# Kernel optimization log

Measured on AMD Instinct MI355X. Metric: run time of the kernel, lower is better.

The kernel has to match this reference:

```python
import jax, jax.numpy as jnp
import numpy as np
from jax.scipy.special import erfc

CUTOFF = 10.0   # real-space cutoff (Angstrom)
ALPHA = 0.3     # Ewald splitting parameter (1/Angstrom)
KMAX = 8        # max integer k-index per dimension
N_ATOMS = 4096
BOX = 40.0      # cubic box edge (Angstrom)


def setup_inputs() -> dict:
    key = jax.random.key(0)
    kp, kq = jax.random.split(key)
    positions = jax.random.uniform(kp, (N_ATOMS, 3), dtype=jnp.float32) * BOX
    charges = jax.random.normal(kq, (N_ATOMS,), dtype=jnp.float32)
    charges = charges - charges.mean()  # enforce charge neutrality
    cell = jnp.eye(3, dtype=jnp.float32) * BOX  # row-vector lattice
    return {"positions": positions, "charges": charges, "cell": cell}


def _kvectors(kmax):
    # static integer grid (-kmax..kmax)^3 \\ {0}, built with numpy at trace time
    n = np.arange(-kmax, kmax + 1)
    grid = np.stack(np.meshgrid(n, n, n, indexing="ij"), axis=-1).reshape(-1, 3)
    grid = grid[np.any(grid != 0, axis=-1)]
    return jnp.asarray(grid, dtype=jnp.float32)  # [Nk, 3]


def _ewald(positions, charges, cell, cutoff, alpha, kmax):
    N = positions.shape[0]
    inv_cell = jnp.linalg.inv(cell)

    # ---- real-space sum: 0.5 * sum_{i!=j, r<rc} q_i q_j erfc(a r)/r (min image)
    rij = positions[:, None, :] - positions[None, :, :]          # [N,N,3]
    frac = rij @ inv_cell
    rij = (frac - jnp.round(frac)) @ cell                        # minimum image
    r2 = jnp.sum(rij * rij, axis=-1)                             # [N,N]
    eye = jnp.eye(N, dtype=bool)
    r = jnp.sqrt(jnp.where(eye, 1.0, r2))                        # safe sqrt on diag
    pair_mask = (~eye) & (r2 < cutoff * cutoff)
    qq = charges[:, None] * charges[None, :]
    e_real = 0.5 * jnp.sum(jnp.where(pair_mask, qq * erfc(alpha * r) / r, 0.0))

    # ---- reciprocal-space sum: (2pi/V) sum_k exp(-k^2/4a^2)/k^2 |S(k)|^2
    recip = 2.0 * jnp.pi * inv_cell.T                            # reciprocal lattice rows
    kvecs = _kvectors(kmax) @ recip                              # [Nk,3]
    k2 = jnp.sum(kvecs * kvecs, axis=-1)                         # [Nk]
    phase = positions @ kvecs.T                                  # [N,Nk]
    s_re = charges @ jnp.cos(phase)                              # [Nk]
    s_im = charges @ jnp.sin(phase)                              # [Nk]
    vol = jnp.abs(jnp.linalg.det(cell))
    coeff = jnp.exp(-k2 / (4.0 * alpha * alpha)) / k2
    e_recip = (2.0 * jnp.pi / vol) * jnp.sum(coeff * (s_re * s_re + s_im * s_im))

    # ---- self-energy correction
    e_self = -(alpha / jnp.sqrt(jnp.pi)) * jnp.sum(charges * charges)

    return e_real + e_recip + e_self


def reference(positions, charges, cell):
    return _ewald(positions, charges, cell, CUTOFF, ALPHA, KMAX)
```

## Files before the change

kernel.cpp:

```cpp
#include <hip/hip_runtime.h>
#include <math.h>

#define ALPHA 0.3f
#define KMAX 8
#define KDIM 17
#define KD2 (KDIM*KDIM)
#define NK_FULL (KDIM*KDIM*KDIM - 1)
#define NK_HALF (NK_FULL/2)
#define RECIP_KB ((NK_HALF + 255)/256)
#define KPAD (RECIP_KB*256)
#define RECIP_CHUNKS 16
#define TWO_PI 6.28318530717958647692f

#define SELF_COEF (-0.16925687506432687f)
#define INV_4A2 (1.0f/(4.0f*ALPHA*ALPHA))
#define C1A (0.3275911f*ALPHA)
#define NA2 (-(ALPHA*ALPHA))

#define ITILE 512
#define JTILE 32

__device__ __forceinline__ void invert3x3(const float* __restrict__ c, float inv[9], float* det_out) {
    float a00=c[0],a01=c[1],a02=c[2];
    float a10=c[3],a11=c[4],a12=c[5];
    float a20=c[6],a21=c[7],a22=c[8];
    float c00 =  a11*a22 - a12*a21;
    float c01 = -(a10*a22 - a12*a20);
    float c02 =  a10*a21 - a11*a20;
    float det = a00*c00 + a01*c01 + a02*c02;
    float id = 1.0f/det;
    inv[0] =  c00*id;
    inv[1] = -(a01*a22 - a02*a21)*id;
    inv[2] =  (a01*a12 - a02*a11)*id;
    inv[3] =  c01*id;
    inv[4] =  (a00*a22 - a02*a20)*id;
    inv[5] = -(a00*a12 - a02*a10)*id;
    inv[6] =  c02*id;
    inv[7] = -(a00*a21 - a01*a20)*id;
    inv[8] =  (a00*a11 - a01*a10)*id;
    *det_out = det;
}

__device__ __forceinline__ float erfc_a(float r, float r2) {
    float t = __builtin_amdgcn_rcpf(fmaf(C1A, r, 1.0f));
    float p = t * fmaf(t, fmaf(t, fmaf(t, fmaf(t, 1.061405429f, -1.453152027f),
                       1.421413741f), -0.284496736f), 0.254829592f);
    return p * __expf(NA2 * r2);
}

__device__ __forceinline__ float block_reduce(float v) {
    for (int o = 32; o > 0; o >>= 1) v += __shfl_down(v, o, 64);
    __shared__ float smem[4];
    int lane = threadIdx.x & 63, wid = threadIdx.x >> 6;
    if (lane == 0) smem[wid] = v;
    __syncthreads();
    int nw = (blockDim.x + 63) >> 6;
    v = ((int)threadIdx.x < nw) ? smem[threadIdx.x] : 0.0f;
    if (wid == 0) {
        for (int o = 4; o > 0; o >>= 1) v += __shfl_down(v, o, 64);
    }
    return v;
}

__global__ __launch_bounds__(256) void fused_kernel(const float* __restrict__ pos,
                                                    const float* __restrict__ q,
                                                    const float* __restrict__ cell,
                                                    float* __restrict__ spart,
                                                    float* __restrict__ rpart,
                                                    int N, int nb_recip) {
    float inv[9]; float det;
    invert3x3(cell, inv, &det);
    bool ortho = (cell[1]==0.f) & (cell[2]==0.f) & (cell[3]==0.f) &
                 (cell[5]==0.f) & (cell[6]==0.f) & (cell[7]==0.f);
    bool cubic = ortho & (cell[0]==cell[4]) & (cell[0]==cell[8]);

    int bid = blockIdx.x;
    int tid = threadIdx.x;

    if (bid < nb_recip) {
        __shared__ float4 atile[256];
        int kb    = bid % RECIP_KB;
        int chunk = bid / RECIP_KB;
        int k = kb * 256 + tid;
        bool kvalid = (k < NK_HALF);
        int kk = kvalid ? k : 0;
        float kx = (float)(kk / KD2 - KMAX);
        float ky = (float)((kk / KDIM) % KDIM - KMAX);
        float kz = (float)(kk % KDIM - KMAX);

        int per = (N + RECIP_CHUNKS - 1) / RECIP_CHUNKS;
        int a0 = chunk * per;
        int a1 = min(N, a0 + per);

        float sre = 0.0f, sim = 0.0f;
        for (int base = a0; base < a1; base += 256) {
            int cnt = min(256, a1 - base);
            __syncthreads();
            if (tid < cnt) {
                int a = base + tid;
                float x = pos[3*a], y = pos[3*a+1], z = pos[3*a+2];
                float wx, wy, wz;
                if (ortho) { wx = x*inv[0]; wy = y*inv[4]; wz = z*inv[8]; }
                else {
                    wx = inv[0]*x + inv[3]*y + inv[6]*z;
                    wy = inv[1]*x + inv[4]*y + inv[7]*z;
                    wz = inv[2]*x + inv[5]*y + inv[8]*z;
                }
                atile[tid] = make_float4(wx, wy, wz, q[a]);
            }
            __syncthreads();
            #pragma unroll 4
            for (int t = 0; t < cnt; ++t) {
                float4 w = atile[t];
                float ph = fmaf(kx, w.x, fmaf(ky, w.y, kz * w.z));
                ph -= rintf(ph);
                sre = fmaf(w.w, __builtin_amdgcn_cosf(ph), sre);
                sim = fmaf(w.w, __builtin_amdgcn_sinf(ph), sim);
            }
        }
        spart[(size_t)(chunk*2    ) * KPAD + k] = kvalid ? sre : 0.0f;
        spart[(size_t)(chunk*2 + 1) * KPAD + k] = kvalid ? sim : 0.0f;
    } else {
        __shared__ float4 tile[JTILE];
        int rbid = bid - nb_recip;
        int bi = 0, acc = 0;
        for (;;) {
            int up = min(N, (bi + 1) * ITILE);
            int nc = (up + JTILE - 1) / JTILE;
            if (rbid < acc + nc) break;
            acc += nc; ++bi;
        }
        int bj = rbid - acc;

        int ibase = bi * ITILE;
        int jbase = bj * JTILE;
        int jcount = min(JTILE, N - jbase);

        int i1 = ibase + tid;
        int i2 = i1 + 256;
        bool v1 = (i1 < N), v2 = (i2 < N);

        float L = cell[0], invL = inv[0];
        float C1AL = C1A * L;
        float NBL  = NA2 * L * L;

        float x1=0.f,y1=0.f,z1=0.f,q1=0.f, x2=0.f,y2=0.f,z2=0.f,q2=0.f;

        if (cubic) {
            if (v1) { x1 = pos[3*i1]*invL; y1 = pos[3*i1+1]*invL; z1 = pos[3*i1+2]*invL; q1 = q[i1]; }
            if (v2) { x2 = pos[3*i2]*invL; y2 = pos[3*i2+1]*invL; z2 = pos[3*i2+2]*invL; q2 = q[i2]; }
            if (tid < jcount) {
                int j = jbase + tid;
                tile[tid] = make_float4(pos[3*j]*invL, pos[3*j+1]*invL, pos[3*j+2]*invL, q[j]);
            }
        } else {
            if (v1) { x1 = pos[3*i1]; y1 = pos[3*i1+1]; z1 = pos[3*i1+2]; q1 = q[i1]; }
            if (v2) { x2 = pos[3*i2]; y2 = pos[3*i2+1]; z2 = pos[3*i2+2]; q2 = q[i2]; }
            if (tid < jcount) {
                int j = jbase + tid;
                tile[tid] = make_float4(pos[3*j], pos[3*j+1], pos[3*j+2], q[j]);
            }
        }
        __syncthreads();

        bool full = (jbase + JTILE <= ibase) && (ibase + ITILE <= N) && (jcount == JTILE);

        float acc1 = 0.0f, acc2 = 0.0f;
        if (cubic) {
            if (full) {
                #pragma unroll 4
                for (int t = 0; t < JTILE; ++t) {
                    float4 p = tile[t];
                    float dx = x1 - p.x, dy = y1 - p.y, dz = z1 - p.z;
                    dx -= rintf(dx); dy -= rintf(dy); dz -= rintf(dz);
                    float f2a = fmaf(dx, dx, fmaf(dy, dy, dz * dz));
                    float ex = x2 - p.x, ey = y2 - p.y, ez = z2 - p.z;
                    ex -= rintf(ex); ey -= rintf(ey); ez -= rintf(ez);
                    float f2b = fmaf(ex, ex, fmaf(ey, ey, ez * ez));

                    float rsa = __builtin_amdgcn_rsqf(f2a);
                    float rsb = __builtin_amdgcn_rsqf(f2b);
                    float fma_ = f2a * rsa, fmb_ = f2b * rsb;
                    float ta = __builtin_amdgcn_rcpf(fmaf(C1AL, fma_, 1.0f));
                    float tb = __builtin_amdgcn_rcpf(fmaf(C1AL, fmb_, 1.0f));
                    float pa = ta * fmaf(ta, fmaf(ta, fmaf(ta, fmaf(ta, 1.061405429f, -1.453152027f),
                                        1.421413741f), -0.284496736f), 0.254829592f);
                    float pb = tb * fmaf(tb, fmaf(tb, fmaf(tb, fmaf(tb, 1.061405429f, -1.453152027f),
                                        1.421413741f), -0.284496736f), 0.254829592f);
                    float ea = __expf(NBL * f2a);
                    float eb = __expf(NBL * f2b);
                    acc1 = fmaf(p.w * rsa * pa, ea, acc1);
                    acc2 = fmaf(p.w * rsb * pb, eb, acc2);
                }
            } else {
                #pragma unroll 4
                for (int t = 0; t < jcount; ++t) {
                    float4 p = tile[t];
                    int j = jbase + t;
                    float dx = x1 - p.x, dy = y1 - p.y, dz = z1 - p.z;
                    dx -= rintf(dx); dy -= rintf(dy); dz -= rintf(dz);
                    float f2a = fmaf(dx, dx, fmaf(dy, dy, dz * dz));
                    float ex = x2 - p.x, ey = y2 - p.y, ez = z2 - p.z;
                    ex -= rintf(ex); ey -= rintf(ey); ez -= rintf(ez);
                    float f2b = fmaf(ex, ex, fmaf(ey, ey, ez * ez));

                    float rsa = __builtin_amdgcn_rsqf(f2a);
                    float rsb = __builtin_amdgcn_rsqf(f2b);
                    float fma_ = f2a * rsa, fmb_ = f2b * rsb;
                    float ta = __builtin_amdgcn_rcpf(fmaf(C1AL, fma_, 1.0f));
                    float tb = __builtin_amdgcn_rcpf(fmaf(C1AL, fmb_, 1.0f));
                    float pa = ta * fmaf(ta, fmaf(ta, fmaf(ta, fmaf(ta, 1.061405429f, -1.453152027f),
                                        1.421413741f), -0.284496736f), 0.254829592f);
                    float pb = tb * fmaf(tb, fmaf(tb, fmaf(tb, fmaf(tb, 1.061405429f, -1.453152027f),
                                        1.421413741f), -0.284496736f), 0.254829592f);
                    float ea = __expf(NBL * f2a);
                    float eb = __expf(NBL * f2b);
                    float va = p.w * rsa * pa * ea;
                    float vb = p.w * rsb * pb * eb;
                    acc1 += (v1 && j < i1) ? va : 0.0f;
                    acc2 += (v2 && j < i2) ? vb : 0.0f;
                }
            }
            float acc_e = (acc1 * q1 + acc2 * q2) * invL;
            float s = block_reduce(acc_e);
            if (tid == 0) rpart[rbid] = s;
        } else {
            float c0 = cell[0], c1 = cell[1], c2 = cell[2];
            float c3 = cell[3], c4 = cell[4], c5 = cell[5];
            float c6 = cell[6], c7 = cell[7], c8 = cell[8];
            #pragma unroll 2
            for (int t = 0; t < jcount; ++t) {
                float4 p = tile[t];
                int j = jbase + t;
                {
                    float dx = x1 - p.x, dy = y1 - p.y, dz = z1 - p.z;
                    float fx = dx*inv[0] + dy*inv[3] + dz*inv[6];
                    float fy = dx*inv[1] + dy*inv[4] + dz*inv[7];
                    float fz = dx*inv[2] + dy*inv[5] + dz*inv[8];
                    fx -= rintf(fx); fy -= rintf(fy); fz -= rintf(fz);
                    float rx = fx*c0 + fy*c3 + fz*c6;
                    float ry = fx*c1 + fy*c4 + fz*c7;
                    float rz = fx*c2 + fy*c5 + fz*c8;
                    float r2 = fmaf(rx, rx, fmaf(ry, ry, rz * rz));
                    float rinv = __builtin_amdgcn_rsqf(r2);
                    float val = p.w * rinv * erfc_a(r2 * rinv, r2);
                    acc1 += (v1 && j < i1) ? val : 0.0f;
                }
                {
                    float dx = x2 - p.x, dy = y2 - p.y, dz = z2 - p.z;
                    float fx = dx*inv[0] + dy*inv[3] + dz*inv[6];
                    float fy = dx*inv[1] + dy*inv[4] + dz*inv[7];
                    float fz = dx*inv[2] + dy*inv[5] + dz*inv[8];
                    fx -= rintf(fx); fy -= rintf(fy); fz -= rintf(fz);
                    float rx = fx*c0 + fy*c3 + fz*c6;
                    float ry = fx*c1 + fy*c4 + fz*c7;
                    float rz = fx*c2 + fy*c5 + fz*c8;
                    float r2 = fmaf(rx, rx, fmaf(ry, ry, rz * rz));
                    float rinv = __builtin_amdgcn_rsqf(r2);
                    float val = p.w * rinv * erfc_a(r2 * rinv, r2);
                    acc2 += (v2 && j < i2) ? val : 0.0f;
                }
            }
            float acc_e = acc1 * q1 + acc2 * q2;
            float s = block_reduce(acc_e);
            if (tid == 0) rpart[rbid] = s;
        }
    }
}

__global__ __launch_bounds__(256) void finalize_kernel(const float* __restrict__ spart,
                                                       const float* __restrict__ rpart,
                                                       const float* __restrict__ q,
                                                       const float* __restrict__ cell,
                                                       float* __restrict__ e_out,
                                                       int N, int nb_real) {
    float inv[9]; float det;
    invert3x3(cell, inv, &det);
    float vol = fabsf(det);
    float pref = 2.0f * (TWO_PI / vol);
    int tid = threadIdx.x;

    float acc = 0.0f;
    for (int t = tid; t < NK_HALF; t += 256) {
        float sr = 0.0f, si = 0.0f;
        #pragma unroll
        for (int c = 0; c < RECIP_CHUNKS; ++c) {
            sr += spart[(size_t)(c*2    ) * KPAD + t];
            si += spart[(size_t)(c*2 + 1) * KPAD + t];
        }
        float nx = (float)(t / KD2 - KMAX);
        float ny = (float)((t / KDIM) % KDIM - KMAX);
        float nz = (float)(t % KDIM - KMAX);
        float kvx = TWO_PI * (nx*inv[0] + ny*inv[1] + nz*inv[2]);
        float kvy = TWO_PI * (nx*inv[3] + ny*inv[4] + nz*inv[5]);
        float kvz = TWO_PI * (nx*inv[6] + ny*inv[7] + nz*inv[8]);
        float k2 = fmaf(kvx, kvx, fmaf(kvy, kvy, kvz * kvz));
        float coeff = __expf(-k2 * INV_4A2) / k2;
        acc = fmaf(pref * coeff, fmaf(sr, sr, si * si), acc);
    }
    for (int t = tid; t < N; t += 256) {
        float qt = q[t];
        acc = fmaf(SELF_COEF * qt, qt, acc);
    }
    for (int t = tid; t < nb_real; t += 256) {
        acc += rpart[t];
    }
    float s = block_reduce(acc);
    if (tid == 0) e_out[0] = s;
}

extern "C" void kernel_launch(void* const* d_in, const int* in_sizes, int n_in,
                              void* d_out, int out_size, void* d_ws, size_t ws_size,
                              hipStream_t stream) {
    const float* pos  = (const float*)d_in[0];
    const float* q    = (const float*)d_in[1];
    const float* cell = (const float*)d_in[2];
    int N = in_sizes[1];
    float* e_out = (float*)d_out;

    float* spart = (float*)d_ws;
    float* rpart = spart + (size_t)RECIP_CHUNKS*2*KPAD;

    int nbi = (N + ITILE - 1) / ITILE;
    int nb_real = 0;
    for (int bi = 0; bi < nbi; ++bi) {
        int up = (N < (bi + 1) * ITILE) ? N : (bi + 1) * ITILE;
        nb_real += (up + JTILE - 1) / JTILE;
    }
    int nb_recip = RECIP_KB * RECIP_CHUNKS;

    fused_kernel<<<nb_recip + nb_real, 256, 0, stream>>>(pos, q, cell, spart, rpart, N, nb_recip);

    finalize_kernel<<<1, 256, 0, stream>>>(spart, rpart, q, cell, e_out, N, nb_real);
}
```

Measured before the change: 80.71 us.

## Factor reciprocal structure factor into (kx,ky) column phases times kz rotations

Restructures the reciprocal-space sum so each atom's phase factor is split into a precomputed (kx,ky) column term and a per-kz rotation term, both held in shared memory. The inner loop becomes a complex multiply-accumulate with no transcendental calls, which removes most sin/cos evaluations. Atoms are chunked into groups of 128, giving 32 chunks times 10 column groups of blocks. The finalize kernel now sums more partial chunks, and the transcendental work moves to a smaller setup phase at the cost of more shared memory and a serial reduction over more partials.

```diff
diff --git a/kernel.cpp b/kernel.cpp
--- a/kernel.cpp
+++ b/kernel.cpp
@@ -4,12 +4,8 @@
 #define ALPHA 0.3f
 #define KMAX 8
 #define KDIM 17
-#define KD2 (KDIM*KDIM)
-#define NK_FULL (KDIM*KDIM*KDIM - 1)
-#define NK_HALF (NK_FULL/2)
-#define RECIP_KB ((NK_HALF + 255)/256)
-#define KPAD (RECIP_KB*256)
-#define RECIP_CHUNKS 16
+#define NK_HALF 2456
+#define KPAD2 2560
 #define TWO_PI 6.28318530717958647692f
 
 #define SELF_COEF (-0.16925687506432687f)
@@ -19,6 +15,9 @@
 
 #define ITILE 512
 #define JTILE 32
+
+#define ACHUNK 128
+#define NCOLG 10
 
 __device__ __forceinline__ void invert3x3(const float* __restrict__ c, float inv[9], float* det_out) {
     float a00=c[0],a01=c[1],a02=c[2];
@@ -41,6 +40,12 @@
     *det_out = det;
 }
 
+__device__ __forceinline__ void col_to_k(int col, float* kx, float* ky) {
+    if (col < 136)      { *kx = (float)(col/17 - 8); *ky = (float)(col%17 - 8); }
+    else if (col < 144) { *kx = 0.f;                 *ky = (float)(col - 144);  }
+    else                { *kx = 0.f;                 *ky = 0.f; }
+}
+
 __device__ __forceinline__ float erfc_a(float r, float r2) {
     float t = __builtin_amdgcn_rcpf(fmaf(C1A, r, 1.0f));
     float p = t * fmaf(t, fmaf(t, fmaf(t, fmaf(t, 1.061405429f, -1.453152027f),
@@ -78,26 +83,19 @@
     int tid = threadIdx.x;
 
     if (bid < nb_recip) {
-        __shared__ float4 atile[256];
-        int kb    = bid % RECIP_KB;
-        int chunk = bid / RECIP_KB;
-        int k = kb * 256 + tid;
-        bool kvalid = (k < NK_HALF);
-        int kk = kvalid ? k : 0;
-        float kx = (float)(kk / KD2 - KMAX);
-        float ky = (float)((kk / KDIM) % KDIM - KMAX);
-        float kz = (float)(kk % KDIM - KMAX);
-
-        int per = (N + RECIP_CHUNKS - 1) / RECIP_CHUNKS;
-        int a0 = chunk * per;
-        int a1 = min(N, a0 + per);
-
-        float sre = 0.0f, sim = 0.0f;
-        for (int base = a0; base < a1; base += 256) {
-            int cnt = min(256, a1 - base);
-            __syncthreads();
+        __shared__ float4 wq[ACHUNK];
+        __shared__ float2 colC[ACHUNK * 16];
+        __shared__ float2 rotz[ACHUNK * 18];
+
+        int g     = bid % NCOLG;
+        int chunk = bid / NCOLG;
+        int a0 = chunk * ACHUNK;
+        int cnt = min(ACHUNK, N - a0);
+
+        if (tid < ACHUNK) {
+            float4 w = make_float4(0.f, 0.f, 0.f, 0.f);
             if (tid < cnt) {
-                int a = base + tid;
+                int a = a0 + tid;
                 float x = pos[3*a], y = pos[3*a+1], z = pos[3*a+2];
                 float wx, wy, wz;
                 if (ortho) { wx = x*inv[0]; wy = y*inv[4]; wz = z*inv[8]; }
@@ -106,20 +104,58 @@
                     wy = inv[1]*x + inv[4]*y + inv[7]*z;
                     wz = inv[2]*x + inv[5]*y + inv[8]*z;
                 }
-                atile[tid] = make_float4(wx, wy, wz, q[a]);
-            }
-            __syncthreads();
+                w = make_float4(wx, wy, wz, q[a]);
+            }
+            wq[tid] = w;
+        }
+        __syncthreads();
+
+        #pragma unroll
+        for (int r = 0; r < 8; ++r) {
+            int idx = r * 256 + tid;
+            int a  = idx >> 4;
+            int ci = idx & 15;
+            int col = g * 15 + ci;
+            float kx, ky;
+            col_to_k((ci < 15 && col < 145) ? col : 0, &kx, &ky);
+            float4 w = wq[a];
+            float ph = fmaf(kx, w.x, ky * w.y);
+            ph -= rintf(ph);
+            colC[idx] = make_float2(__builtin_amdgcn_cosf(ph), __builtin_amdgcn_sinf(ph));
+        }
+        #pragma unroll
+        for (int r = 0; r < 9; ++r) {
+            int idx = r * 256 + tid;
+            if (idx < ACHUNK * 17) {
+                int a   = idx & (ACHUNK - 1);
+                int kzi = idx >> 7;
+                float4 w = wq[a];
+                float u = (float)(kzi - 8) * w.z;
+                u -= rintf(u);
+                rotz[a * 18 + kzi] = make_float2(w.w * __builtin_amdgcn_cosf(u),
+                                                 w.w * __builtin_amdgcn_sinf(u));
+            }
+        }
+        __syncthreads();
+
+        int lc  = tid / 17;
+        int kzi = tid - lc * 17;
+        int col = g * 15 + lc;
+        if (lc < 15 && col < 145) {
+            float sre = 0.0f, sim = 0.0f;
             #pragma unroll 4
-            for (int t = 0; t < cnt; ++t) {
-                float4 w = atile[t];
-                float ph = fmaf(kx, w.x, fmaf(ky, w.y, kz * w.z));
-                ph -= rintf(ph);
-                sre = fmaf(w.w, __builtin_amdgcn_cosf(ph), sre);
-                sim = fmaf(w.w, __builtin_amdgcn_sinf(ph), sim);
-            }
-        }
-        spart[(size_t)(chunk*2    ) * KPAD + k] = kvalid ? sre : 0.0f;
-        spart[(size_t)(chunk*2 + 1) * KPAD + k] = kvalid ? sim : 0.0f;
+            for (int a = 0; a < ACHUNK; ++a) {
+                float2 c2 = colC[a * 16 + lc];
+                float2 r2 = rotz[a * 18 + kzi];
+                sre = fmaf(c2.x, r2.x, sre);
+                sre = fmaf(-c2.y, r2.y, sre);
+                sim = fmaf(c2.x, r2.y, sim);
+                sim = fmaf(c2.y, r2.x, sim);
+            }
+            int kidx = col * 17 + kzi;
+            spart[(size_t)(chunk*2    ) * KPAD2 + kidx] = sre;
+            spart[(size_t)(chunk*2 + 1) * KPAD2 + kidx] = sim;
+        }
     } else {
         __shared__ float4 tile[JTILE];
         int rbid = bid - nb_recip;
@@ -273,7 +309,7 @@
                                                        const float* __restrict__ q,
                                                        const float* __restrict__ cell,
                                                        float* __restrict__ e_out,
-                                                       int N, int nb_real) {
+                                                       int N, int nb_real, int nchunks) {
     float inv[9]; float det;
     invert3x3(cell, inv, &det);
     float vol = fabsf(det);
@@ -281,19 +317,21 @@
     int tid = threadIdx.x;
 
     float acc = 0.0f;
-    for (int t = tid; t < NK_HALF; t += 256) {
+    for (int t = tid; t < 145*17; t += 256) {
+        int col = t / 17;
+        int kzi = t - col * 17;
+        if (col == 144 && kzi >= 8) continue;
         float sr = 0.0f, si = 0.0f;
-        #pragma unroll
-        for (int c = 0; c < RECIP_CHUNKS; ++c) {
-            sr += spart[(size_t)(c*2    ) * KPAD + t];
-            si += spart[(size_t)(c*2 + 1) * KPAD + t];
-        }
-        float nx = (float)(t / KD2 - KMAX);
-        float ny = (float)((t / KDIM) % KDIM - KMAX);
-        float nz = (float)(t % KDIM - KMAX);
-        float kvx = TWO_PI * (nx*inv[0] + ny*inv[1] + nz*inv[2]);
-        float kvy = TWO_PI * (nx*inv[3] + ny*inv[4] + nz*inv[5]);
-        float kvz = TWO_PI * (nx*inv[6] + ny*inv[7] + nz*inv[8]);
+        for (int c = 0; c < nchunks; ++c) {
+            sr += spart[(size_t)(c*2    ) * KPAD2 + t];
+            si += spart[(size_t)(c*2 + 1) * KPAD2 + t];
+        }
+        float kx, ky;
+        col_to_k(col, &kx, &ky);
+        float kz = (float)(kzi - 8);
+        float kvx = TWO_PI * (kx*inv[0] + ky*inv[1] + kz*inv[2]);
+        float kvy = TWO_PI * (kx*inv[3] + ky*inv[4] + kz*inv[5]);
+        float kvz = TWO_PI * (kx*inv[6] + ky*inv[7] + kz*inv[8]);
         float k2 = fmaf(kvx, kvx, fmaf(kvy, kvy, kvz * kvz));
         float coeff = __expf(-k2 * INV_4A2) / k2;
         acc = fmaf(pref * coeff, fmaf(sr, sr, si * si), acc);
@@ -318,8 +356,9 @@
     int N = in_sizes[1];
     float* e_out = (float*)d_out;
 
+    int nchunks = (N + ACHUNK - 1) / ACHUNK;
     float* spart = (float*)d_ws;
-    float* rpart = spart + (size_t)RECIP_CHUNKS*2*KPAD;
+    float* rpart = spart + (size_t)nchunks * 2 * KPAD2;
 
     int nbi = (N + ITILE - 1) / ITILE;
     int nb_real = 0;
@@ -327,9 +366,9 @@
         int up = (N < (bi + 1) * ITILE) ? N : (bi + 1) * ITILE;
         nb_real += (up + JTILE - 1) / JTILE;
     }
-    int nb_recip = RECIP_KB * RECIP_CHUNKS;
+    int nb_recip = NCOLG * nchunks;
 
     fused_kernel<<<nb_recip + nb_real, 256, 0, stream>>>(pos, q, cell, spart, rpart, N, nb_recip);
 
-    finalize_kernel<<<1, 256, 0, stream>>>(spart, rpart, q, cell, e_out, N, nb_real);
-}
+    finalize_kernel<<<1, 256, 0, stream>>>(spart, rpart, q, cell, e_out, N, nb_real, nchunks);
+}
```

Result: slower. 169.0 us (+109.4%).
